# Kernel optimization log

Measured on AMD Instinct MI355X. Metric: run time of the kernel, lower is better.

The kernel has to match this reference:

```python
import jax, jax.numpy as jnp
import numpy as np

HEAD_DIM = 64
EMBED_DIM = 1024


def setup_inputs() -> dict:
    key = jax.random.key(0)
    k0, k1, k2, k3, k4, k5, k6 = jax.random.split(key, 7)
    B, T = 4, 2048
    s = 1.0 / np.sqrt(EMBED_DIM)
    return {
        "inputs": jax.random.normal(k0, (B, T, EMBED_DIM), dtype=jnp.float32),
        "Wq": jax.random.uniform(k1, (HEAD_DIM, EMBED_DIM), jnp.float32, -s, s),
        "bq": jax.random.uniform(k2, (HEAD_DIM,), jnp.float32, -s, s),
        "Wk": jax.random.uniform(k3, (HEAD_DIM, EMBED_DIM), jnp.float32, -s, s),
        "bk": jax.random.uniform(k4, (HEAD_DIM,), jnp.float32, -s, s),
        "Wv": jax.random.uniform(k5, (HEAD_DIM, EMBED_DIM), jnp.float32, -s, s),
        "bv": jax.random.uniform(k6, (HEAD_DIM,), jnp.float32, -s, s),
    }


def reference(inputs, Wq, bq, Wk, bk, Wv, bv):
    # inputs: [B, T, E]
    q = jnp.einsum("bte,he->bth", inputs, Wq) + bq  # [B, T, H]
    k = jnp.einsum("bte,he->bth", inputs, Wk) + bk
    v = jnp.einsum("bte,he->bth", inputs, Wv) + bv
    scores = jnp.einsum("bth,bsh->bts", q, k)  # [B, T, T]
    T = scores.shape[-1]
    causal = jnp.tril(jnp.ones((T, T), dtype=bool))  # True = keep
    scores = jnp.where(causal, scores, -jnp.inf)
    weights = jax.nn.softmax(scores / jnp.sqrt(jnp.float32(HEAD_DIM)), axis=-1)
    # dropout is identity in eval mode
    return jnp.einsum("bts,bsh->bth", weights, v)
```

## Files before the change

### kernel.cpp

```cpp
#include <hip/hip_runtime.h>
#include <hip/hip_bf16.h>

#define BATCH 4
#define SEQ   2048
#define EMB   1024
#define HD    64
#define BT    (BATCH * SEQ)
#define XS_STRIDE 1040

#define QSCALE 0.18033688011112042f

typedef __attribute__((ext_vector_type(8))) short bf16x8;
typedef __attribute__((ext_vector_type(4))) float f32x4;

__device__ __forceinline__ ushort f2bf(float f) {
    unsigned u = __float_as_uint(f);
    return (ushort)((u + 0x7FFFu + ((u >> 16) & 1u)) >> 16);
}

__global__ __launch_bounds__(256) void prep(
    const float* __restrict__ Wq, const float* __restrict__ bq,
    const float* __restrict__ Wk, const float* __restrict__ bk,
    const float* __restrict__ Wv, const float* __restrict__ bv,
    ushort* __restrict__ Wf, float* __restrict__ bb)
{
    const int fid = (int)blockIdx.x * 256 + (int)threadIdx.x;
    const int kc   = fid / 768;
    const int rem  = fid - kc * 768;
    const int sub  = rem >> 6;
    const int lane = rem & 63;
    const int row  = (sub & 3) * 16 + (lane & 15);
    const int e0   = kc * 32 + (lane >> 4) * 8;
    const float* W = (sub < 4) ? Wq : ((sub < 8) ? Wk : Wv);
    const float4 a0 = *(const float4*)(W + (size_t)row * EMB + e0);
    const float4 a1 = *(const float4*)(W + (size_t)row * EMB + e0 + 4);
    bf16x8 w;
    w[0] = (short)f2bf(a0.x); w[1] = (short)f2bf(a0.y);
    w[2] = (short)f2bf(a0.z); w[3] = (short)f2bf(a0.w);
    w[4] = (short)f2bf(a1.x); w[5] = (short)f2bf(a1.y);
    w[6] = (short)f2bf(a1.z); w[7] = (short)f2bf(a1.w);
    *(bf16x8*)(Wf + (size_t)fid * 8) = w;
    if (blockIdx.x == 0 && threadIdx.x < 192) {
        const int i = (int)threadIdx.x;
        const float* B = (i < 64) ? bq : ((i < 128) ? bk : bv);
        bb[i] = B[i & 63];
    }
}

__global__ __launch_bounds__(256) void qkv_gemm(
    const float* __restrict__ x, const ushort* __restrict__ Wf,
    const float* __restrict__ bb,
    ushort* __restrict__ Qf, ushort* __restrict__ Kf, ushort* __restrict__ Vf)
{
    const int t0   = (int)blockIdx.x * 16;
    const int tid  = (int)threadIdx.x;
    const int wv   = tid >> 6;
    const int lane = tid & 63;
    const int col  = lane & 15, quad = lane >> 4;

    __shared__ ushort xs[16][XS_STRIDE];

    #pragma unroll 4
    for (int it = 0; it < 16; ++it) {
        const int idx = it * 256 + tid;
        const int row = idx >> 8, c4 = idx & 255;
        const float4 v = *(const float4*)(x + (size_t)(t0 + row) * EMB + c4 * 4);
        ushort4 pk;
        pk.x = f2bf(v.x); pk.y = f2bf(v.y); pk.z = f2bf(v.z); pk.w = f2bf(v.w);
        *(ushort4*)&xs[row][c4 * 4] = pk;
    }
    __syncthreads();

    f32x4 acc[3];
    #pragma unroll
    for (int s = 0; s < 3; ++s) acc[s] = (f32x4){0.f, 0.f, 0.f, 0.f};
    const int sub0 = wv * 3;

    #pragma unroll 8
    for (int kc = 0; kc < 32; ++kc) {
        const bf16x8 a = *(const bf16x8*)&xs[col][kc * 32 + quad * 8];
        #pragma unroll
        for (int s = 0; s < 3; ++s) {
            const bf16x8 w = *(const bf16x8*)(Wf + ((size_t)(kc * 12 + sub0 + s) * 64 + lane) * 8);
            acc[s] = __builtin_amdgcn_mfma_f32_16x16x32_bf16(a, w, acc[s], 0, 0, 0);
        }
    }

    const int b  = t0 >> 11;
    const int qt = (t0 >> 4) & 127;
    const int sg = t0 + quad * 4;
    const int itk = (sg & (SEQ - 1)) >> 6;
    #pragma unroll
    for (int s = 0; s < 3; ++s) {
        const int sub  = sub0 + s;
        const int hrow = sub * 16 + col;
        const float bias = bb[hrow];
        if (sub < 4) {
            const int h = hrow;
            const int f = h >> 5, qd = (h >> 3) & 3, j = h & 7;
            ushort* base = Qf + (((size_t)(b * 128 + qt) * 2 + f) * 64 + qd * 16 + quad * 4) * 8 + j;
            #pragma unroll
            for (int i = 0; i < 4; ++i)
                base[i * 8] = f2bf((acc[s][i] + bias) * QSCALE);
        } else if (sub < 8) {
            const int h = hrow - 64;
            const int f = h >> 5, qd = (h >> 3) & 3, j = h & 7;
            const size_t frag = ((size_t)(b * 32 + itk) * 4 + ((sg >> 4) & 3)) * 2 + f;
            ushort* base = Kf + frag * 512 + ((size_t)((sg & 15) + 16 * qd)) * 8 + j;
            #pragma unroll
            for (int i = 0; i < 4; ++i)
                base[i * 8] = f2bf(acc[s][i] + bias);
        } else {
            const int h = hrow - 128;
            const int k0 = sg & 63;
            const int f = k0 >> 5, qd = (k0 >> 3) & 3, j0 = k0 & 7;
            const size_t frag = ((size_t)(b * 32 + itk) * 4 + (h >> 4)) * 2 + f;
            ushort4 pk;
            pk.x = f2bf(acc[s][0] + bias); pk.y = f2bf(acc[s][1] + bias);
            pk.z = f2bf(acc[s][2] + bias); pk.w = f2bf(acc[s][3] + bias);
            *(ushort4*)(Vf + frag * 512 + ((size_t)((h & 15) + 16 * qd)) * 8 + j0) = pk;
        }
    }
}

__global__ __launch_bounds__(64, 3) void attn_part(
    const ushort* __restrict__ Qf, const ushort* __restrict__ Kf,
    const ushort* __restrict__ Vf,
    float* __restrict__ pl, float* __restrict__ pO)
{
    const int idx  = (int)blockIdx.x;
    const int j    = idx & 7;
    const int rest = idx >> 3;
    const int b    = rest & 3;
    const int tile = 127 - (rest >> 2);
    const int t0   = tile * 16;
    const int nt   = (tile >> 2) + 1;
    const int lane = (int)threadIdx.x;
    const int col  = lane & 15, quad = lane >> 4;

    const ushort* Qb = Qf + ((size_t)(b * 128 + tile) * 2) * 512;
    const bf16x8 aq0 = *(const bf16x8*)(Qb + (size_t)lane * 8);
    const bf16x8 aq1 = *(const bf16x8*)(Qb + 512 + (size_t)lane * 8);

    float l_r[4];
    f32x4 o[4];
    #pragma unroll
    for (int i = 0; i < 4; ++i) { l_r[i] = 0.f; o[i] = (f32x4){0.f,0.f,0.f,0.f}; }

    __shared__ ushort pt[16][80];

    bf16x8 kc[4][2];
    {
        const ushort* Kt = Kf + ((size_t)(b * 32 + j) * 8) * 512;
        #pragma unroll
        for (int sub = 0; sub < 4; ++sub) {
            kc[sub][0] = *(const bf16x8*)(Kt + (size_t)(sub * 2 + 0) * 512 + (size_t)lane * 8);
            kc[sub][1] = *(const bf16x8*)(Kt + (size_t)(sub * 2 + 1) * 512 + (size_t)lane * 8);
        }
    }

    for (int it = j; it < nt; it += 8) {
        const int s0 = it * 64;
        const bool hasNext = (it + 8 < nt);

        f32x4 sc[4];
        #pragma unroll
        for (int sub = 0; sub < 4; ++sub) {
            f32x4 z = {0.f, 0.f, 0.f, 0.f};
            z = __builtin_amdgcn_mfma_f32_16x16x32_bf16(aq0, kc[sub][0], z, 0, 0, 0);
            z = __builtin_amdgcn_mfma_f32_16x16x32_bf16(aq1, kc[sub][1], z, 0, 0, 0);
            sc[sub] = z;
        }

        bf16x8 kn[4][2], vf[4][2];
        {
            const ushort* Vt = Vf + ((size_t)(b * 32 + it) * 8) * 512;
            #pragma unroll
            for (int sub = 0; sub < 4; ++sub) {
                vf[sub][0] = *(const bf16x8*)(Vt + (size_t)(sub * 2 + 0) * 512 + (size_t)lane * 8);
                vf[sub][1] = *(const bf16x8*)(Vt + (size_t)(sub * 2 + 1) * 512 + (size_t)lane * 8);
            }
        }
        if (hasNext) {
            const ushort* Kt = Kf + ((size_t)(b * 32 + it + 8) * 8) * 512;
            #pragma unroll
            for (int sub = 0; sub < 4; ++sub) {
                kn[sub][0] = *(const bf16x8*)(Kt + (size_t)(sub * 2 + 0) * 512 + (size_t)lane * 8);
                kn[sub][1] = *(const bf16x8*)(Kt + (size_t)(sub * 2 + 1) * 512 + (size_t)lane * 8);
            }
        }

        if (it == nt - 1) {
            #pragma unroll
            for (int sub = 0; sub < 4; ++sub)
                #pragma unroll
                for (int i = 0; i < 4; ++i) {
                    const int s = s0 + sub * 16 + col, t = t0 + quad * 4 + i;
                    if (s > t) sc[sub][i] = -1e30f;
                }
        }

        #pragma unroll
        for (int sub = 0; sub < 4; ++sub)
            #pragma unroll
            for (int i = 0; i < 4; ++i) {
                const float p = exp2f(sc[sub][i]);
                l_r[i] += p;
                pt[quad * 4 + i][sub * 16 + col] = f2bf(p);
            }

        __asm__ volatile("s_waitcnt lgkmcnt(0)" ::: "memory");
        const bf16x8 ap0 = *(const bf16x8*)&pt[col][quad * 8];
        const bf16x8 ap1 = *(const bf16x8*)&pt[col][32 + quad * 8];

        #pragma unroll
        for (int sub = 0; sub < 4; ++sub) {
            o[sub] = __builtin_amdgcn_mfma_f32_16x16x32_bf16(ap0, vf[sub][0], o[sub], 0, 0, 0);
            o[sub] = __builtin_amdgcn_mfma_f32_16x16x32_bf16(ap1, vf[sub][1], o[sub], 0, 0, 0);
        }

        if (hasNext) {
            #pragma unroll
            for (int sub = 0; sub < 4; ++sub) { kc[sub][0] = kn[sub][0]; kc[sub][1] = kn[sub][1]; }
        }
    }

    #pragma unroll
    for (int d = 1; d < 16; d <<= 1)
        #pragma unroll
        for (int i = 0; i < 4; ++i) l_r[i] += __shfl_xor(l_r[i], d, 64);

    const size_t base = ((size_t)(b * 128 + tile)) * 8 + j;
    float* Op = pO + base * 1024;
    #pragma unroll
    for (int sub = 0; sub < 4; ++sub)
        #pragma unroll
        for (int i = 0; i < 4; ++i)
            Op[(quad * 4 + i) * 64 + sub * 16 + col] = o[sub][i];
    if (col == 0) {
        #pragma unroll
        for (int i = 0; i < 4; ++i)
            pl[base * 16 + quad * 4 + i] = l_r[i];
    }
}

__global__ __launch_bounds__(256) void attn_merge(
    const float* __restrict__ pl, const float* __restrict__ pO,
    float* __restrict__ out)
{
    const int blk = (int)blockIdx.x;
    const int b = blk >> 7, t0 = (blk & 127) * 16;
    const int tid = (int)threadIdx.x;
    const int row = tid >> 4, c0 = (tid & 15) * 4;
    const size_t base = (size_t)blk * 8;

    float ls = 0.f;
    float4 r = {0.f, 0.f, 0.f, 0.f};
    #pragma unroll
    for (int j = 0; j < 8; ++j) {
        ls += pl[(base + j) * 16 + row];
        const float4 O = *(const float4*)&pO[(base + j) * 1024 + row * 64 + c0];
        r.x += O.x; r.y += O.y; r.z += O.z; r.w += O.w;
    }
    const float rinv = 1.0f / ls;
    float4 res = {r.x * rinv, r.y * rinv, r.z * rinv, r.w * rinv};
    *(float4*)(out + ((size_t)b * SEQ + t0 + row) * HD + c0) = res;
}

extern "C" void kernel_launch(void* const* d_in, const int* in_sizes, int n_in,
                              void* d_out, int out_size, void* d_ws, size_t ws_size,
                              hipStream_t stream)
{
    const float* x  = (const float*)d_in[0];
    const float* Wq = (const float*)d_in[1];
    const float* bq = (const float*)d_in[2];
    const float* Wk = (const float*)d_in[3];
    const float* bk = (const float*)d_in[4];
    const float* Wv = (const float*)d_in[5];
    const float* bv = (const float*)d_in[6];
    float* out = (float*)d_out;

    char* ws = (char*)d_ws;
    ushort* Wf  = (ushort*)(ws);
    float*  bb  = (float*)(ws + 0x60000);
    ushort* Qfb = (ushort*)(ws + 0x61000);
    ushort* Kfb = (ushort*)(ws + 0x161000);
    ushort* Vfb = (ushort*)(ws + 0x261000);
    float*  plb = (float*)(ws + 0x440000);
    float*  pOb = (float*)(ws + 0x480000);

    prep<<<96, 256, 0, stream>>>(Wq, bq, Wk, bk, Wv, bv, Wf, bb);
    qkv_gemm<<<BT / 16, 256, 0, stream>>>(x, Wf, bb, Qfb, Kfb, Vfb);
    attn_part<<<4096, 64, 0, stream>>>(Qfb, Kfb, Vfb, plb, pOb);
    attn_merge<<<512, 256, 0, stream>>>(plb, pOb, out);
}
```

Before: 112.4 us.

## Fuse split-KV attention partials and merge into one workgroup via LDS

Replaces the 8-way split-KV attention kernel plus a separate merge kernel with a single kernel where 4 wavefronts in one 256-thread block each process a strided quarter of the key tiles. The wavefronts then combine their partial outputs and row sums through shared memory and write the normalized result directly. This removes one kernel launch and the global round trip of partial O and l buffers. In exchange it cuts the KV split from 8 to 4, which halves the parallel slices available for the long causal rows, and it adds more LDS per block plus a block-wide barrier.

```diff
diff --git a/kernel.cpp b/kernel.cpp
--- a/kernel.cpp
+++ b/kernel.cpp
@@ -123,19 +123,18 @@
     }
 }
 
-__global__ __launch_bounds__(64, 3) void attn_part(
+__global__ __launch_bounds__(256) void attn(
     const ushort* __restrict__ Qf, const ushort* __restrict__ Kf,
-    const ushort* __restrict__ Vf,
-    float* __restrict__ pl, float* __restrict__ pO)
-{
-    const int idx  = (int)blockIdx.x;
-    const int j    = idx & 7;
-    const int rest = idx >> 3;
-    const int b    = rest & 3;
-    const int tile = 127 - (rest >> 2);
+    const ushort* __restrict__ Vf, float* __restrict__ out)
+{
+    const int blk  = (int)blockIdx.x;
+    const int b    = blk & 3;
+    const int tile = 127 - (blk >> 2);
     const int t0   = tile * 16;
     const int nt   = (tile >> 2) + 1;
-    const int lane = (int)threadIdx.x;
+    const int tid  = (int)threadIdx.x;
+    const int j    = tid >> 6;
+    const int lane = tid & 63;
     const int col  = lane & 15, quad = lane >> 4;
 
     const ushort* Qb = Qf + ((size_t)(b * 128 + tile) * 2) * 512;
@@ -147,10 +146,12 @@
     #pragma unroll
     for (int i = 0; i < 4; ++i) { l_r[i] = 0.f; o[i] = (f32x4){0.f,0.f,0.f,0.f}; }
 
-    __shared__ ushort pt[16][80];
+    __shared__ ushort pt[4][16][80];
+    __shared__ __align__(16) float op[4][16][68];
+    __shared__ float ll[4][16];
 
     bf16x8 kc[4][2];
-    {
+    if (j < nt) {
         const ushort* Kt = Kf + ((size_t)(b * 32 + j) * 8) * 512;
         #pragma unroll
         for (int sub = 0; sub < 4; ++sub) {
@@ -159,9 +160,9 @@
         }
     }
 
-    for (int it = j; it < nt; it += 8) {
+    for (int it = j; it < nt; it += 4) {
         const int s0 = it * 64;
-        const bool hasNext = (it + 8 < nt);
+        const bool hasNext = (it + 4 < nt);
 
         f32x4 sc[4];
         #pragma unroll
@@ -182,7 +183,7 @@
             }
         }
         if (hasNext) {
-            const ushort* Kt = Kf + ((size_t)(b * 32 + it + 8) * 8) * 512;
+            const ushort* Kt = Kf + ((size_t)(b * 32 + it + 4) * 8) * 512;
             #pragma unroll
             for (int sub = 0; sub < 4; ++sub) {
                 kn[sub][0] = *(const bf16x8*)(Kt + (size_t)(sub * 2 + 0) * 512 + (size_t)lane * 8);
@@ -206,12 +207,12 @@
             for (int i = 0; i < 4; ++i) {
                 const float p = exp2f(sc[sub][i]);
                 l_r[i] += p;
-                pt[quad * 4 + i][sub * 16 + col] = f2bf(p);
+                pt[j][quad * 4 + i][sub * 16 + col] = f2bf(p);
             }
 
         __asm__ volatile("s_waitcnt lgkmcnt(0)" ::: "memory");
-        const bf16x8 ap0 = *(const bf16x8*)&pt[col][quad * 8];
-        const bf16x8 ap1 = *(const bf16x8*)&pt[col][32 + quad * 8];
+        const bf16x8 ap0 = *(const bf16x8*)&pt[j][col][quad * 8];
+        const bf16x8 ap1 = *(const bf16x8*)&pt[j][col][32 + quad * 8];
 
         #pragma unroll
         for (int sub = 0; sub < 4; ++sub) {
@@ -230,41 +231,33 @@
         #pragma unroll
         for (int i = 0; i < 4; ++i) l_r[i] += __shfl_xor(l_r[i], d, 64);
 
-    const size_t base = ((size_t)(b * 128 + tile)) * 8 + j;
-    float* Op = pO + base * 1024;
     #pragma unroll
     for (int sub = 0; sub < 4; ++sub)
         #pragma unroll
         for (int i = 0; i < 4; ++i)
-            Op[(quad * 4 + i) * 64 + sub * 16 + col] = o[sub][i];
+            op[j][quad * 4 + i][sub * 16 + col] = o[sub][i];
     if (col == 0) {
         #pragma unroll
         for (int i = 0; i < 4; ++i)
-            pl[base * 16 + quad * 4 + i] = l_r[i];
-    }
-}
-
-__global__ __launch_bounds__(256) void attn_merge(
-    const float* __restrict__ pl, const float* __restrict__ pO,
-    float* __restrict__ out)
-{
-    const int blk = (int)blockIdx.x;
-    const int b = blk >> 7, t0 = (blk & 127) * 16;
-    const int tid = (int)threadIdx.x;
-    const int row = tid >> 4, c0 = (tid & 15) * 4;
-    const size_t base = (size_t)blk * 8;
-
-    float ls = 0.f;
-    float4 r = {0.f, 0.f, 0.f, 0.f};
-    #pragma unroll
-    for (int j = 0; j < 8; ++j) {
-        ls += pl[(base + j) * 16 + row];
-        const float4 O = *(const float4*)&pO[(base + j) * 1024 + row * 64 + c0];
-        r.x += O.x; r.y += O.y; r.z += O.z; r.w += O.w;
-    }
-    const float rinv = 1.0f / ls;
-    float4 res = {r.x * rinv, r.y * rinv, r.z * rinv, r.w * rinv};
-    *(float4*)(out + ((size_t)b * SEQ + t0 + row) * HD + c0) = res;
+            ll[j][quad * 4 + i] = l_r[i];
+    }
+    __syncthreads();
+
+    {
+        const int row = tid >> 4, c0 = (tid & 15) * 4;
+        const float4 p0 = *(const float4*)&op[0][row][c0];
+        const float4 p1 = *(const float4*)&op[1][row][c0];
+        const float4 p2 = *(const float4*)&op[2][row][c0];
+        const float4 p3 = *(const float4*)&op[3][row][c0];
+        const float ls = ll[0][row] + ll[1][row] + ll[2][row] + ll[3][row];
+        const float rinv = 1.0f / ls;
+        float4 res;
+        res.x = (p0.x + p1.x + p2.x + p3.x) * rinv;
+        res.y = (p0.y + p1.y + p2.y + p3.y) * rinv;
+        res.z = (p0.z + p1.z + p2.z + p3.z) * rinv;
+        res.w = (p0.w + p1.w + p2.w + p3.w) * rinv;
+        *(float4*)(out + ((size_t)b * SEQ + t0 + row) * HD + c0) = res;
+    }
 }
 
 extern "C" void kernel_launch(void* const* d_in, const int* in_sizes, int n_in,
@@ -286,11 +279,8 @@
     ushort* Qfb = (ushort*)(ws + 0x61000);
     ushort* Kfb = (ushort*)(ws + 0x161000);
     ushort* Vfb = (ushort*)(ws + 0x261000);
-    float*  plb = (float*)(ws + 0x440000);
-    float*  pOb = (float*)(ws + 0x480000);
 
     prep<<<96, 256, 0, stream>>>(Wq, bq, Wk, bk, Wv, bv, Wf, bb);
     qkv_gemm<<<BT / 16, 256, 0, stream>>>(x, Wf, bb, Qfb, Kfb, Vfb);
-    attn_part<<<4096, 64, 0, stream>>>(Qfb, Kfb, Vfb, plb, pOb);
-    attn_merge<<<512, 256, 0, stream>>>(plb, pOb, out);
-}
+    attn<<<512, 256, 0, stream>>>(Qfb, Kfb, Vfb, out);
+}
```

After: 109.0 us. -3.1%, faster.
